# Kernel tuning notes

Hardware: AMD Instinct MI355X
Metric: run time of the kernel (lower is better)

The kernel has to match this reference:

```python
import jax, jax.numpy as jnp
import numpy as np


def _entropy_of_rounded(vals):
    """Entropy (base 2) of the empirical distribution of unique rounded values.

    Equivalent to torch.unique(torch.round(v), return_counts=True) followed by
    -sum(c/N * log2(c/N)). Implemented jit-compatibly via sort + run-length counts.
    """
    n = vals.shape[0]
    s = jnp.sort(jnp.round(vals))
    is_new = jnp.concatenate([jnp.ones((1,), dtype=bool), s[1:] != s[:-1]])
    seg = jnp.cumsum(is_new.astype(jnp.int32)) - 1  # run id per element
    counts = jax.ops.segment_sum(jnp.ones_like(s, dtype=jnp.float32), seg, num_segments=n)
    p = counts / n
    safe_p = jnp.where(counts > 0, p, 1.0)
    return -jnp.sum(jnp.where(counts > 0, p * jnp.log2(safe_p), 0.0))


def _forward(x, key):
    b = x.shape[0]
    temp = x.reshape(b, -1)  # [B, D]
    d = temp.shape[1]

    # torch.corrcoef over rows of temp -> [B, B]
    xc = temp - jnp.mean(temp, axis=1, keepdims=True)
    cov = xc @ xc.T  # [B, B]; scale cancels in correlation
    diag = jnp.diag(cov)
    corr = cov / jnp.sqrt(diag[:, None] * diag[None, :])

    # batch mean over rows and per-row mse vs it
    temp_mean = jnp.mean(temp, axis=0)  # [D]
    row_mse = jnp.mean(jnp.square(temp - temp_mean[None, :]), axis=1)  # [B]
    total_mse = jnp.sum(row_mse)

    # entropies of rounded values: whole batch and per row
    batch_entropy = _entropy_of_rounded(temp.reshape(-1))
    row_ents = jax.lax.map(_entropy_of_rounded, temp)  # [B], sequential to bound memory

    factor1 = jnp.mean(jnp.abs(corr), axis=1)  # [B]
    factor2 = row_mse / total_mse  # [B]
    ratio = row_ents / batch_entropy
    factor3 = jnp.minimum(ratio, 1.0 / ratio)  # if ratio > 1: 1/ratio
    p = (1.0 - factor1) * factor2 * factor3  # [B]

    # per-row Bernoulli mask: rand > p_i  (keep prob = 1 - p_i)
    u = jax.random.uniform(key, x.shape, dtype=x.dtype)
    p_b = p.reshape((b,) + (1,) * (x.ndim - 1))
    mask = (u > p_b).astype(x.dtype)

    # faithful to source: rescale uses the LAST row's p only
    return mask * x / (1.0 - p[-1])


def setup_inputs() -> dict:
    key = jax.random.key(0)
    x = jax.random.normal(key, (64, 256, 56, 56), dtype=jnp.float32)
    return {"x": x, "module": 0}


def reference(x, module):
    # `module` is accepted but unused, matching the original forward signature.
    return _forward(x, jax.random.key(42))
```

## Files before the change

kernel.cpp:

```cpp
#include <hip/hip_runtime.h>
#include <stdint.h>

#define NROWS 64
#define DCOLS 802816
#define NTOT  51380224u
#define NBLK  784
#define BCOLS 1024

__device__ __forceinline__ void threefry2x32_k42(uint32_t x0, uint32_t x1,
                                                 uint32_t& r0, uint32_t& r1) {
  const uint32_t ks0 = 0u, ks1 = 42u, ks2 = 0x1BD11BF0u;
  x0 += ks0; x1 += ks1;
#define TF_ROT(v, r) (((v) << (r)) | ((v) >> (32 - (r))))
#define TF_RND(r) { x0 += x1; x1 = TF_ROT(x1, r); x1 ^= x0; }
  TF_RND(13) TF_RND(15) TF_RND(26) TF_RND(6)
  x0 += ks1; x1 += ks2 + 1u;
  TF_RND(17) TF_RND(29) TF_RND(16) TF_RND(24)
  x0 += ks2; x1 += ks0 + 2u;
  TF_RND(13) TF_RND(15) TF_RND(26) TF_RND(6)
  x0 += ks0; x1 += ks1 + 3u;
  TF_RND(17) TF_RND(29) TF_RND(16) TF_RND(24)
  x0 += ks1; x1 += ks2 + 4u;
  TF_RND(13) TF_RND(15) TF_RND(26) TF_RND(6)
  x0 += ks2; x1 += ks0 + 5u;
  r0 = x0; r1 = x1;
#undef TF_RND
#undef TF_ROT
}

__global__ __launch_bounds__(256) void k_stats(const float* __restrict__ x,
                                               float* __restrict__ gpart,
                                               float* __restrict__ rpart,
                                               int* __restrict__ hpart) {
  __shared__ float tile[64 * 128];
  __shared__ int   hist[64 * 64];
  __shared__ float rsumLDS[64];
  const int t = threadIdx.x;
  const int b = blockIdx.x;
  for (int o = t; o < 4096; o += 256) hist[o] = 0;
  if (t < 64) rsumLDS[t] = 0.f;

  float acc[8][8];
#pragma unroll
  for (int a = 0; a < 8; a++)
#pragma unroll
    for (int c = 0; c < 8; c++) acc[a][c] = 0.f;
  float rsum[8] = {0.f, 0.f, 0.f, 0.f, 0.f, 0.f, 0.f, 0.f};

  const int kq = t >> 6;
  const int ti = t & 7;
  const int tj = (t >> 3) & 7;
  const int sg = t & 31;
  const int rowgrp = t >> 5;
  const int rep = sg & 3;

  const float* srcbase = x + (size_t)b * BCOLS;
  float4 R[8];
#pragma unroll
  for (int rr = 0; rr < 8; rr++) {
    const int row = rr * 8 + rowgrp;
    R[rr] = *(const float4*)(srcbase + (size_t)row * DCOLS + sg * 4);
  }

  for (int sl = 0; sl < 8; ++sl) {
    __syncthreads();
#pragma unroll
    for (int rr = 0; rr < 8; rr++) {
      const int row = rr * 8 + rowgrp;
      *(float4*)(&tile[row * 128 + ((sg ^ (row & 7)) << 2)]) = R[rr];
    }
#pragma unroll
    for (int rr = 0; rr < 8; rr++) {
      const int row = rr * 8 + rowgrp;
      const float4 v = R[rr];
      rsum[rr] += (v.x + v.y) + (v.z + v.w);
      int* hrow = &hist[row << 6];
      atomicAdd(&hrow[(min(max((int)rintf(v.x) + 8, 0), 15) << 2) + rep], 1);
      atomicAdd(&hrow[(min(max((int)rintf(v.y) + 8, 0), 15) << 2) + rep], 1);
      atomicAdd(&hrow[(min(max((int)rintf(v.z) + 8, 0), 15) << 2) + rep], 1);
      atomicAdd(&hrow[(min(max((int)rintf(v.w) + 8, 0), 15) << 2) + rep], 1);
    }
    if (sl < 7) {
      const float* src = srcbase + (size_t)(sl + 1) * 128;
#pragma unroll
      for (int rr = 0; rr < 8; rr++) {
        const int row = rr * 8 + rowgrp;
        R[rr] = *(const float4*)(src + (size_t)row * DCOLS + sg * 4);
      }
    }
    __syncthreads();
    for (int kk = 0; kk < 8; ++kk) {
      const int g = kq * 8 + kk;
      float4 av[8], bv[8];
#pragma unroll
      for (int a = 0; a < 8; a++)
        av[a] = *(const float4*)(&tile[(a * 8 + ti) * 128 + ((g ^ ti) << 2)]);
#pragma unroll
      for (int c = 0; c < 8; c++)
        bv[c] = *(const float4*)(&tile[(c * 8 + tj) * 128 + ((g ^ tj) << 2)]);
#pragma unroll
      for (int a = 0; a < 8; a++)
#pragma unroll
        for (int c = 0; c < 8; c++)
          acc[a][c] += av[a].x * bv[c].x + av[a].y * bv[c].y +
                       av[a].z * bv[c].z + av[a].w * bv[c].w;
    }
  }
#pragma unroll
  for (int rr = 0; rr < 8; rr++)
    atomicAdd(&rsumLDS[rr * 8 + rowgrp], rsum[rr]);

  const int tiled = ti + 8 * tj;
  __syncthreads();
  if (kq & 1) {
#pragma unroll
    for (int a = 0; a < 8; a++)
#pragma unroll
      for (int c = 0; c < 8; c++)
        tile[(kq >> 1) * 4096 + tiled * 64 + a * 8 + c] = acc[a][c];
  }
  __syncthreads();
  if (!(kq & 1)) {
#pragma unroll
    for (int a = 0; a < 8; a++)
#pragma unroll
      for (int c = 0; c < 8; c++)
        acc[a][c] += tile[(kq >> 1) * 4096 + tiled * 64 + a * 8 + c];
  }
  __syncthreads();
  if (kq == 2) {
#pragma unroll
    for (int a = 0; a < 8; a++)
#pragma unroll
      for (int c = 0; c < 8; c++)
        tile[tiled * 64 + a * 8 + c] = acc[a][c];
  }
  __syncthreads();
  if (kq == 0) {
    float* gp = gpart + (size_t)b * 4096 + tiled * 64;
#pragma unroll
    for (int a = 0; a < 8; a++)
#pragma unroll
      for (int c = 0; c < 8; c++)
        gp[a * 8 + c] = acc[a][c] + tile[tiled * 64 + a * 8 + c];
  }
  if (t < 64) rpart[(size_t)b * 64 + t] = rsumLDS[t];
  for (int o = t; o < 1024; o += 256) {
    const int* h = &hist[((o >> 4) << 6) + ((o & 15) << 2)];
    hpart[(size_t)b * 1024 + o] = (h[0] + h[1]) + (h[2] + h[3]);
  }
}

__global__ __launch_bounds__(256) void k_reduce(const float* __restrict__ gpart,
                                                const float* __restrict__ rpart,
                                                const int* __restrict__ hpart,
                                                double* __restrict__ G,
                                                double* __restrict__ S,
                                                int* __restrict__ HIST) {
  __shared__ double red[4][64];
  const int t = threadIdx.x;
  const int ol = t & 63, q = t >> 6;
  const int o = blockIdx.x * 64 + ol;
  double acc = 0.0;
  if (o < 4096) {
    for (int i = 0; i < 196; i++)
      acc += (double)gpart[(size_t)(q * 196 + i) * 4096 + o];
  } else if (o < 4160) {
    const int r = o - 4096;
    for (int i = 0; i < 196; i++)
      acc += (double)rpart[(size_t)(q * 196 + i) * 64 + r];
  } else {
    const int h = o - 4160;
    long long ia = 0;
    for (int i = 0; i < 196; i++)
      ia += hpart[(size_t)(q * 196 + i) * 1024 + h];
    acc = (double)ia;
  }
  red[q][ol] = acc;
  __syncthreads();
  if (q == 0) {
    const double tot = ((red[0][ol] + red[1][ol]) + red[2][ol]) + red[3][ol];
    if (o < 4096) {
      const int tileIdx = o >> 6, e = o & 63;
      const int ti = tileIdx & 7, tj = tileIdx >> 3, a = e >> 3, c = e & 7;
      G[(a * 8 + ti) * 64 + (c * 8 + tj)] = tot;
    } else if (o < 4160) {
      S[o - 4096] = tot;
    } else {
      HIST[o - 4160] = (int)tot;
    }
  }
}

__global__ void k_finalize(const double* __restrict__ G,
                           const double* __restrict__ S,
                           const int* __restrict__ HIST,
                           unsigned* __restrict__ mth, float* __restrict__ scl) {
#pragma clang fp contract(off)
  __shared__ double sp_sh[64];
  __shared__ float rm_sh[64];
  __shared__ float p_sh[64];
  const int i = threadIdx.x;
  const double invD = 1.0 / 802816.0;
  const double Si = S[i];
  const float di = (float)(G[i * 64 + i] - Si * Si * invD);
  float f1sum = 0.0f;
  for (int j = 0; j < 64; j++) {
    const double Sj = S[j];
    const float c = (float)(G[i * 64 + j] - Si * Sj * invD);
    const float dj = (float)(G[j * 64 + j] - Sj * Sj * invD);
    const float r = c / sqrtf(di * dj);
    f1sum = f1sum + fabsf(r);
  }
  const float f1 = f1sum / 64.0f;
  double sp = 0;
  for (int j = 0; j < 64; j++) sp += G[i * 64 + j];
  sp_sh[i] = sp; __syncthreads();
  double T = 0;
  for (int j = 0; j < 64; j++) T += sp_sh[j];
  const double rm = (G[i * 64 + i] - sp * (2.0 / 64.0) + T * (1.0 / 4096.0)) * invD;
  rm_sh[i] = (float)rm; __syncthreads();
  float tot = 0.f;
  for (int j = 0; j < 64; j++) tot = tot + rm_sh[j];
  const float f2 = rm_sh[i] / tot;
  const float LN2F = 0.69314718055994530942f;
  float Hb = 0.f;
  for (int k = 0; k < 16; k++) {
    int c = 0;
    for (int r = 0; r < 64; r++) c += HIST[r * 16 + k];
    if (c > 0) {
      const float cf = (float)(c > 16777216 ? 16777216 : c);
      const float pk = cf / 51380224.0f;
      const float lg = (float)log((double)pk) / LN2F;
      Hb = Hb + pk * lg;
    }
  }
  Hb = -Hb;
  float Hr = 0.f;
  for (int k = 0; k < 16; k++) {
    const int c = HIST[i * 16 + k];
    if (c > 0) {
      const float pk = ((float)c) / 802816.0f;
      const float lg = (float)log((double)pk) / LN2F;
      Hr = Hr + pk * lg;
    }
  }
  Hr = -Hr;
  const float ratio = Hr / Hb;
  const float f3 = fminf(ratio, 1.0f / ratio);
  const float p = ((1.0f - f1) * f2) * f3;
  p_sh[i] = p; __syncthreads();
  mth[i] = (unsigned)floor((double)p * 8388608.0);
  if (i == 0) {
    const float scale = 1.0f - p_sh[63];
    scl[0] = (float)(1.0 / (double)scale);
  }
}

__global__ __launch_bounds__(256) void k_mask(const float* __restrict__ x,
                                              float* __restrict__ out,
                                              const unsigned* __restrict__ mth,
                                              const float* __restrict__ scl) {
  const float s = scl[0];
  const unsigned base = ((unsigned)blockIdx.x * 256u + threadIdx.x) * 4u;
  const unsigned row = base / (unsigned)DCOLS;
  const unsigned th = mth[row];
  const float4 v = *(const float4*)(x + base);
  float res[4];
  const float vv[4] = {v.x, v.y, v.z, v.w};
#pragma unroll
  for (int e = 0; e < 4; e++) {
    const unsigned idx = base + (unsigned)e;
    uint32_t r0, r1;
    threefry2x32_k42(0u, idx, r0, r1);
    const uint32_t bits = r0 ^ r1;
    const bool keep = (bits >> 9) > th;
    res[e] = keep ? vv[e] * s : 0.0f;
  }
  float4 o; o.x = res[0]; o.y = res[1]; o.z = res[2]; o.w = res[3];
  *(float4*)(out + base) = o;
}

extern "C" void kernel_launch(void* const* d_in, const int* in_sizes, int n_in,
                              void* d_out, int out_size, void* d_ws, size_t ws_size,
                              hipStream_t stream) {
  const float* x = (const float*)d_in[0];
  float* out = (float*)d_out;
  char* ws = (char*)d_ws;
  float*  gpart = (float*)(ws);
  float*  rpart = (float*)(ws + 12845056);
  int*    hpart = (int*)(ws + 13045760);
  double* G     = (double*)(ws + 16257024);
  double* S     = (double*)(ws + 16289792);
  int*    HIST  = (int*)(ws + 16290304);
  unsigned* MTH = (unsigned*)(ws + 16294400);
  float*  SCL   = (float*)(ws + 16294656);

  k_stats<<<NBLK, 256, 0, stream>>>(x, gpart, rpart, hpart);
  k_reduce<<<81, 256, 0, stream>>>(gpart, rpart, hpart, G, S, HIST);
  k_finalize<<<1, 64, 0, stream>>>(G, S, HIST, MTH, SCL);
  k_mask<<<NTOT / 1024u, 256, 0, stream>>>(x, out, MTH, SCL);
}
```

Measured before the change: 578.1 us.

## Compute Gram matrix with bf16x3 split MFMA instead of scalar FP32 FMAs

```diff
diff --git a/kernel.cpp b/kernel.cpp
--- a/kernel.cpp
+++ b/kernel.cpp
@@ -6,6 +6,10 @@
 #define NTOT  51380224u
 #define NBLK  784
 #define BCOLS 1024
+#define NSLICE 8
+
+typedef short short8v __attribute__((ext_vector_type(8)));
+typedef float f32x4 __attribute__((ext_vector_type(4)));
 
 __device__ __forceinline__ void threefry2x32_k42(uint32_t x0, uint32_t x1,
                                                  uint32_t& r0, uint32_t& r1) {
@@ -28,11 +32,17 @@
 #undef TF_ROT
 }
 
+__device__ __forceinline__ uint32_t bf16_rne(float x) {
+  const uint32_t u = __float_as_uint(x);
+  return (u + 0x7FFFu + ((u >> 16) & 1u)) >> 16;
+}
+
 __global__ __launch_bounds__(256) void k_stats(const float* __restrict__ x,
                                                float* __restrict__ gpart,
                                                float* __restrict__ rpart,
                                                int* __restrict__ hpart) {
-  __shared__ float tile[64 * 128];
+  __shared__ short Ht[64 * 128];
+  __shared__ short Lt[64 * 128];
   __shared__ int   hist[64 * 64];
   __shared__ float rsumLDS[64];
   const int t = threadIdx.x;
@@ -40,19 +50,20 @@
   for (int o = t; o < 4096; o += 256) hist[o] = 0;
   if (t < 64) rsumLDS[t] = 0.f;
 
-  float acc[8][8];
-#pragma unroll
-  for (int a = 0; a < 8; a++)
-#pragma unroll
-    for (int c = 0; c < 8; c++) acc[a][c] = 0.f;
-  float rsum[8] = {0.f, 0.f, 0.f, 0.f, 0.f, 0.f, 0.f, 0.f};
-
-  const int kq = t >> 6;
-  const int ti = t & 7;
-  const int tj = (t >> 3) & 7;
+  const int w = t >> 6;
+  const int lane = t & 63;
+  const int i0 = (w & 1) * 2;
+  const int j0 = (w >> 1) * 2;
   const int sg = t & 31;
   const int rowgrp = t >> 5;
-  const int rep = sg & 3;
+  const int rep = t & 3;
+
+  f32x4 acc[2][2];
+#pragma unroll
+  for (int ui = 0; ui < 2; ui++)
+#pragma unroll
+    for (int uj = 0; uj < 2; uj++) acc[ui][uj] = (f32x4)0.f;
+  float rsum[8] = {0.f, 0.f, 0.f, 0.f, 0.f, 0.f, 0.f, 0.f};
 
   const float* srcbase = x + (size_t)b * BCOLS;
   float4 R[8];
@@ -62,13 +73,8 @@
     R[rr] = *(const float4*)(srcbase + (size_t)row * DCOLS + sg * 4);
   }
 
-  for (int sl = 0; sl < 8; ++sl) {
+  for (int sl = 0; sl < NSLICE; ++sl) {
     __syncthreads();
-#pragma unroll
-    for (int rr = 0; rr < 8; rr++) {
-      const int row = rr * 8 + rowgrp;
-      *(float4*)(&tile[row * 128 + ((sg ^ (row & 7)) << 2)]) = R[rr];
-    }
 #pragma unroll
     for (int rr = 0; rr < 8; rr++) {
       const int row = rr * 8 + rowgrp;
@@ -79,8 +85,20 @@
       atomicAdd(&hrow[(min(max((int)rintf(v.y) + 8, 0), 15) << 2) + rep], 1);
       atomicAdd(&hrow[(min(max((int)rintf(v.z) + 8, 0), 15) << 2) + rep], 1);
       atomicAdd(&hrow[(min(max((int)rintf(v.w) + 8, 0), 15) << 2) + rep], 1);
-    }
-    if (sl < 7) {
+      const uint32_t hx = bf16_rne(v.x), hy = bf16_rne(v.y);
+      const uint32_t hz = bf16_rne(v.z), hw = bf16_rne(v.w);
+      const uint32_t lx = bf16_rne(v.x - __uint_as_float(hx << 16));
+      const uint32_t ly = bf16_rne(v.y - __uint_as_float(hy << 16));
+      const uint32_t lz = bf16_rne(v.z - __uint_as_float(hz << 16));
+      const uint32_t lw = bf16_rne(v.w - __uint_as_float(hw << 16));
+      uint2 hp, lp;
+      hp.x = hx | (hy << 16); hp.y = hz | (hw << 16);
+      lp.x = lx | (ly << 16); lp.y = lz | (lw << 16);
+      const int woff = row * 256 + ((((sg >> 1) ^ (row & 7)) << 4) | ((sg & 1) << 3));
+      *(uint2*)((char*)Ht + woff) = hp;
+      *(uint2*)((char*)Lt + woff) = lp;
+    }
+    if (sl + 1 < NSLICE) {
       const float* src = srcbase + (size_t)(sl + 1) * 128;
 #pragma unroll
       for (int rr = 0; rr < 8; rr++) {
@@ -89,61 +107,48 @@
       }
     }
     __syncthreads();
-    for (int kk = 0; kk < 8; ++kk) {
-      const int g = kq * 8 + kk;
-      float4 av[8], bv[8];
-#pragma unroll
-      for (int a = 0; a < 8; a++)
-        av[a] = *(const float4*)(&tile[(a * 8 + ti) * 128 + ((g ^ ti) << 2)]);
-#pragma unroll
-      for (int c = 0; c < 8; c++)
-        bv[c] = *(const float4*)(&tile[(c * 8 + tj) * 128 + ((g ^ tj) << 2)]);
-#pragma unroll
-      for (int a = 0; a < 8; a++)
-#pragma unroll
-        for (int c = 0; c < 8; c++)
-          acc[a][c] += av[a].x * bv[c].x + av[a].y * bv[c].y +
-                       av[a].z * bv[c].z + av[a].w * bv[c].w;
+#pragma unroll
+    for (int ks = 0; ks < 4; ks++) {
+      const int kc = ks * 4 + (lane >> 4);
+      short8v aH[2], aL[2], bH[2], bL[2];
+#pragma unroll
+      for (int u = 0; u < 2; u++) {
+        const int ar = (i0 + u) * 16 + (lane & 15);
+        const int aoff = ar * 256 + ((kc ^ (ar & 7)) << 4);
+        aH[u] = *(short8v*)((char*)Ht + aoff);
+        aL[u] = *(short8v*)((char*)Lt + aoff);
+        const int br = (j0 + u) * 16 + (lane & 15);
+        const int boff = br * 256 + ((kc ^ (br & 7)) << 4);
+        bH[u] = *(short8v*)((char*)Ht + boff);
+        bL[u] = *(short8v*)((char*)Lt + boff);
+      }
+#pragma unroll
+      for (int ui = 0; ui < 2; ui++)
+#pragma unroll
+        for (int uj = 0; uj < 2; uj++) {
+          acc[ui][uj] = __builtin_amdgcn_mfma_f32_16x16x32_bf16(aH[ui], bH[uj], acc[ui][uj], 0, 0, 0);
+          acc[ui][uj] = __builtin_amdgcn_mfma_f32_16x16x32_bf16(aH[ui], bL[uj], acc[ui][uj], 0, 0, 0);
+          acc[ui][uj] = __builtin_amdgcn_mfma_f32_16x16x32_bf16(aL[ui], bH[uj], acc[ui][uj], 0, 0, 0);
+          acc[ui][uj] = __builtin_amdgcn_mfma_f32_16x16x32_bf16(aL[ui], bL[uj], acc[ui][uj], 0, 0, 0);
+        }
     }
   }
 #pragma unroll
   for (int rr = 0; rr < 8; rr++)
     atomicAdd(&rsumLDS[rr * 8 + rowgrp], rsum[rr]);
 
-  const int tiled = ti + 8 * tj;
+  float* gp = gpart + (size_t)b * 4096;
+#pragma unroll
+  for (int ui = 0; ui < 2; ui++)
+#pragma unroll
+    for (int uj = 0; uj < 2; uj++)
+#pragma unroll
+      for (int r = 0; r < 4; r++) {
+        const int grow = (i0 + ui) * 16 + (lane >> 4) * 4 + r;
+        const int gcol = (j0 + uj) * 16 + (lane & 15);
+        gp[grow * 64 + gcol] = acc[ui][uj][r];
+      }
   __syncthreads();
-  if (kq & 1) {
-#pragma unroll
-    for (int a = 0; a < 8; a++)
-#pragma unroll
-      for (int c = 0; c < 8; c++)
-        tile[(kq >> 1) * 4096 + tiled * 64 + a * 8 + c] = acc[a][c];
-  }
-  __syncthreads();
-  if (!(kq & 1)) {
-#pragma unroll
-    for (int a = 0; a < 8; a++)
-#pragma unroll
-      for (int c = 0; c < 8; c++)
-        acc[a][c] += tile[(kq >> 1) * 4096 + tiled * 64 + a * 8 + c];
-  }
-  __syncthreads();
-  if (kq == 2) {
-#pragma unroll
-    for (int a = 0; a < 8; a++)
-#pragma unroll
-      for (int c = 0; c < 8; c++)
-        tile[tiled * 64 + a * 8 + c] = acc[a][c];
-  }
-  __syncthreads();
-  if (kq == 0) {
-    float* gp = gpart + (size_t)b * 4096 + tiled * 64;
-#pragma unroll
-    for (int a = 0; a < 8; a++)
-#pragma unroll
-      for (int c = 0; c < 8; c++)
-        gp[a * 8 + c] = acc[a][c] + tile[tiled * 64 + a * 8 + c];
-  }
   if (t < 64) rpart[(size_t)b * 64 + t] = rsumLDS[t];
   for (int o = t; o < 1024; o += 256) {
     const int* h = &hist[((o >> 4) << 6) + ((o & 15) << 2)];
@@ -181,9 +186,7 @@
   if (q == 0) {
     const double tot = ((red[0][ol] + red[1][ol]) + red[2][ol]) + red[3][ol];
     if (o < 4096) {
-      const int tileIdx = o >> 6, e = o & 63;
-      const int ti = tileIdx & 7, tj = tileIdx >> 3, a = e >> 3, c = e & 7;
-      G[(a * 8 + ti) * 64 + (c * 8 + tj)] = tot;
+      G[o] = tot;
     } else if (o < 4160) {
       S[o - 4096] = tot;
     } else {
```

Measured after the change: 484.0 us. 16.3% less time.
